# Performance work log

Hardware: AMD Instinct MI355X
Metric: run time of the kernel (lower is better)

## Reference

```python
import jax, jax.numpy as jnp
import numpy as np

D_MODEL = 1024
N_HEADS = 16
DEPTH = D_MODEL // N_HEADS
B, S = 2, 2048


def layer_norm(x, gamma, beta):
    # Faithful to the torch module: unbiased std (ddof=1), eps added to std.
    mean = jnp.mean(x, axis=-1, keepdims=True)
    std = jnp.std(x, axis=-1, ddof=1, keepdims=True)
    return gamma * ((x - mean) / (std + 1e-6)) + beta


def setup_inputs() -> dict:
    key = jax.random.key(0)
    ks = jax.random.split(key, 12)
    sc = 0.02
    x = jax.random.normal(ks[0], (B, S, D_MODEL), jnp.float32)
    mask = jnp.triu(jnp.ones((S, S), jnp.float32), k=1)  # 1 where masked (future)
    return {
        "x": x,
        "mask": mask,
        "wq_w": jax.random.normal(ks[1], (D_MODEL, D_MODEL), jnp.float32) * sc,
        "wq_b": jnp.zeros((D_MODEL,), jnp.float32),
        "wk_w": jax.random.normal(ks[2], (D_MODEL, D_MODEL), jnp.float32) * sc,
        "wk_b": jnp.zeros((D_MODEL,), jnp.float32),
        "wv_w": jax.random.normal(ks[3], (D_MODEL, D_MODEL), jnp.float32) * sc,
        "wv_b": jnp.zeros((D_MODEL,), jnp.float32),
        "dense_w": jax.random.normal(ks[4], (D_MODEL, D_MODEL), jnp.float32) * sc,
        "dense_b": jnp.zeros((D_MODEL,), jnp.float32),
        "gamma1": jnp.ones((D_MODEL,), jnp.float32),
        "beta1": jnp.zeros((D_MODEL,), jnp.float32),
        "gamma2": jnp.ones((D_MODEL,), jnp.float32),
        "beta2": jnp.zeros((D_MODEL,), jnp.float32),
        "fc_w": jax.random.normal(ks[5], (4 * D_MODEL, D_MODEL), jnp.float32) * sc,
        "proj_w": jax.random.normal(ks[6], (D_MODEL, 4 * D_MODEL), jnp.float32) * sc,
    }


def reference(x, mask, wq_w, wq_b, wk_w, wk_b, wv_w, wv_b, dense_w, dense_b,
              gamma1, beta1, gamma2, beta2, fc_w, proj_w):
    # x: [B,S,D]. Dropout is identity in eval.
    xn = layer_norm(x, gamma1, beta1)

    def split(h):  # [B,S,D] -> [B,H,S,depth]
        return h.reshape(B, S, N_HEADS, DEPTH).transpose(0, 2, 1, 3)

    q = split(xn @ wq_w.T + wq_b)
    k = split(xn @ wk_w.T + wk_b)
    v = split(xn @ wv_w.T + wv_b)

    scores = jnp.einsum("bhqd,bhkd->bhqk", q, k) / jnp.sqrt(
        jnp.asarray(DEPTH, jnp.float32))
    scores = scores + mask * -1e9
    attn = jax.nn.softmax(scores, axis=-1)
    ctx = jnp.einsum("bhqk,bhkd->bhqd", attn, v)
    ctx = ctx.transpose(0, 2, 1, 3).reshape(B, S, D_MODEL)
    attn_out = ctx @ dense_w.T + dense_b

    # Residual adds the *normed* x (faithful to the original ordering).
    h = xn + attn_out
    hn = layer_norm(h, gamma2, beta2)

    ff = jax.nn.gelu(hn @ fc_w.T, approximate=False) @ proj_w.T
    return hn + ff
```

## Files before the change

kernel.cpp:

```cpp
#include <hip/hip_runtime.h>
#include <math.h>

typedef __bf16 bf16;
typedef __attribute__((ext_vector_type(2))) __bf16 bf16x2;
typedef __attribute__((ext_vector_type(4))) __bf16 bf16x4;
typedef __attribute__((ext_vector_type(8))) __bf16 bf16x8;
typedef __attribute__((ext_vector_type(4))) float f32x4;

#define D_MODEL 1024
#define NH 16
#define DP 64
#define BB 2
#define SEQ 2048
#define TOK 4096
#define FFD 4096
#define AST 72

__device__ __forceinline__ void async16(bf16* lds, const bf16* g) {
    __builtin_amdgcn_global_load_lds(
        (__attribute__((address_space(1))) void*)g,
        (__attribute__((address_space(3))) void*)lds, 16, 0, 0);
}

__device__ __forceinline__ f32x4 mfma16(bf16x8 a, bf16x8 b, f32x4 c) {
    return __builtin_amdgcn_mfma_f32_16x16x32_bf16(a, b, c, 0, 0, 0);
}

__device__ __forceinline__ void xcd_swz(int& bx, int& by, int& bz) {
    const int gx = gridDim.x, gy = gridDim.y;
    const int nwg = gx * gy * gridDim.z;
    const int orig = (blockIdx.z * gy + blockIdx.y) * gx + blockIdx.x;
    const int q = nwg >> 3;
    const int n = (orig & 7) * q + (orig >> 3);
    bx = n % gx;
    const int r = n / gx;
    by = r % gy;
    bz = r / gy;
}

struct CvtArgs {
    const float4* in[6];
    bf16x4* out[6];
};
__global__ __launch_bounds__(256) void cvt_all(CvtArgs a)
{
    const int i = blockIdx.x * 256 + threadIdx.x;
    int seg, idx;
    if (i < (1 << 20)) { seg = i >> 18; idx = i & ((1 << 18) - 1); }
    else {
        const int j = i - (1 << 20);
        seg = 4 + (j >> 20); idx = j & ((1 << 20) - 1);
    }
    const float4 v = a.in[seg][idx];
    bf16x4 o; o[0] = (bf16)v.x; o[1] = (bf16)v.y; o[2] = (bf16)v.z; o[3] = (bf16)v.w;
    a.out[seg][idx] = o;
}

template<typename TIN>
__global__ __launch_bounds__(256) void ln_kernel(
    const TIN* __restrict__ in, const float* __restrict__ g,
    const float* __restrict__ be, bf16* __restrict__ out)
{
    const size_t row = blockIdx.x;
    const int t = threadIdx.x;
    const TIN* x = in + row * D_MODEL;

    float v0, v1, v2, v3;
    if constexpr (sizeof(TIN) == 4) {
        const float4 xv = *(const float4*)(x + t * 4);
        v0 = xv.x; v1 = xv.y; v2 = xv.z; v3 = xv.w;
    } else {
        const bf16x4 xv = *(const bf16x4*)(x + t * 4);
        v0 = (float)xv[0]; v1 = (float)xv[1]; v2 = (float)xv[2]; v3 = (float)xv[3];
    }
    float s  = v0 + v1 + v2 + v3;
    float ss = v0*v0 + v1*v1 + v2*v2 + v3*v3;
    #pragma unroll
    for (int off = 32; off > 0; off >>= 1) {
        s  += __shfl_down(s, off);
        ss += __shfl_down(ss, off);
    }
    __shared__ float rs[4], rss[4];
    if ((t & 63) == 0) { rs[t >> 6] = s; rss[t >> 6] = ss; }
    __syncthreads();
    const float S  = rs[0] + rs[1] + rs[2] + rs[3];
    const float SS = rss[0] + rss[1] + rss[2] + rss[3];
    const float mean = S * (1.0f / 1024.0f);
    const float var  = fmaxf((SS - S * mean) * (1.0f / 1023.0f), 0.0f);
    const float inv  = 1.0f / (sqrtf(var) + 1e-6f);

    const float4 gv = *(const float4*)(g  + t * 4);
    const float4 bv = *(const float4*)(be + t * 4);
    bf16x4 ov;
    ov[0] = (bf16)(gv.x * ((v0 - mean) * inv) + bv.x);
    ov[1] = (bf16)(gv.y * ((v1 - mean) * inv) + bv.y);
    ov[2] = (bf16)(gv.z * ((v2 - mean) * inv) + bv.z);
    ov[3] = (bf16)(gv.w * ((v3 - mean) * inv) + bv.w);
    *(bf16x4*)(out + row * D_MODEL + t * 4) = ov;
}

template<int EPI, typename TOUT>
__global__ __launch_bounds__(256, 2) void gemm_bt(
    const bf16* __restrict__ A, const bf16* __restrict__ W,
    const float* __restrict__ bias, const bf16* res,
    TOUT* C, int M, int N, int K, float scale)
{
    int bx, by, bz; xcd_swz(bx, by, bz);
    __shared__ __align__(16) bf16 As[2][128 * 32];
    __shared__ __align__(16) bf16 Bs[2][128 * 32];
    const int t = threadIdx.x;
    const int w = t >> 6, lane = t & 63;
    const int fr = lane & 15, quad = lane >> 4;
    const int m0 = by * 128, n0 = bx * 128;
    const int wm = (w >> 1) * 64, wn = (w & 1) * 64;

    const f32x4 z = {0.f, 0.f, 0.f, 0.f};
    f32x4 acc[4][4];
    #pragma unroll
    for (int i = 0; i < 4; ++i)
        #pragma unroll
        for (int j = 0; j < 4; ++j) acc[i][j] = z;

    const int nk = K >> 5;
    const int srow = t >> 2, ssub = t & 3;

    #pragma unroll
    for (int call = 0; call < 2; ++call) {
        const int row = call * 64 + srow;
        async16(&As[0][(size_t)(call * 256 + w * 64) * 8],
                A + (size_t)(m0 + row) * K + ssub * 8);
        async16(&Bs[0][(size_t)(call * 256 + w * 64) * 8],
                W + (size_t)(n0 + row) * K + ssub * 8);
    }
    __syncthreads();

    for (int kt = 0; kt < nk; ++kt) {
        const int cur = kt & 1;
        if (kt + 1 < nk) {
            const int k0 = (kt + 1) << 5;
            #pragma unroll
            for (int call = 0; call < 2; ++call) {
                const int row = call * 64 + srow;
                async16(&As[cur ^ 1][(size_t)(call * 256 + w * 64) * 8],
                        A + (size_t)(m0 + row) * K + k0 + ssub * 8);
                async16(&Bs[cur ^ 1][(size_t)(call * 256 + w * 64) * 8],
                        W + (size_t)(n0 + row) * K + k0 + ssub * 8);
            }
        }
        bf16x8 af[4], bfr[4];
        #pragma unroll
        for (int i = 0; i < 4; ++i)
            af[i] = *(const bf16x8*)&As[cur][(wm + i * 16 + fr) * 32 + quad * 8];
        #pragma unroll
        for (int j = 0; j < 4; ++j)
            bfr[j] = *(const bf16x8*)&Bs[cur][(wn + j * 16 + fr) * 32 + quad * 8];
        #pragma unroll
        for (int i = 0; i < 4; ++i)
            #pragma unroll
            for (int j = 0; j < 4; ++j)
                acc[i][j] = mfma16(af[i], bfr[j], acc[i][j]);
        __syncthreads();
    }

    #pragma unroll
    for (int i = 0; i < 4; ++i) {
        #pragma unroll
        for (int j = 0; j < 4; ++j) {
            #pragma unroll
            for (int r = 0; r < 4; ++r) {
                const int m = m0 + wm + i * 16 + quad * 4 + r;
                const int n = n0 + wn + j * 16 + fr;
                float v = acc[i][j][r];
                if (EPI == 1) {
                    v += bias[n];
                    v += (float)res[(size_t)m * N + n];
                    C[(size_t)m * N + n] = (TOUT)v;
                } else if (EPI == 2) {
                    v = 0.5f * v * (1.0f + erff(v * 0.70710678118f));
                    C[(size_t)m * N + n] = (TOUT)v;
                } else {
                    v += (float)res[(size_t)m * N + n];
                    C[(size_t)m * N + n] = (TOUT)v;
                }
            }
        }
    }
}

template<int EPI, typename TOUT>
__global__ __launch_bounds__(256, 2) void gemm_bt64(
    const bf16* __restrict__ A, const bf16* __restrict__ W,
    const float* __restrict__ bias, const bf16* res,
    TOUT* C, TOUT* Cb, int M, int N, int K, int kchunk)
{
    int bx, by, bz; xcd_swz(bx, by, bz);
    __shared__ __align__(16) bf16 As[2][128 * 32];
    __shared__ __align__(16) bf16 Bs[2][64 * 32];
    const int t = threadIdx.x;
    const int w = t >> 6, lane = t & 63;
    const int fr = lane & 15, quad = lane >> 4;
    const int m0 = by * 128, n0 = bx * 64;
    const int kbase = bz * kchunk;
    TOUT* Cz = (EPI == 4 && bz) ? Cb : C;
    const int wm = (w >> 1) * 64, wn = (w & 1) * 32;

    const f32x4 z = {0.f, 0.f, 0.f, 0.f};
    f32x4 acc[4][2];
    #pragma unroll
    for (int i = 0; i < 4; ++i)
        #pragma unroll
        for (int j = 0; j < 2; ++j) acc[i][j] = z;

    const int nk = kchunk >> 5;
    const int srow = t >> 2, ssub = t & 3;

    #pragma unroll
    for (int call = 0; call < 2; ++call) {
        const int row = call * 64 + srow;
        async16(&As[0][(size_t)(call * 256 + w * 64) * 8],
                A + (size_t)(m0 + row) * K + kbase + ssub * 8);
    }
    async16(&Bs[0][(size_t)(w * 64) * 8],
            W + (size_t)(n0 + srow) * K + kbase + ssub * 8);
    __syncthreads();

    for (int kt = 0; kt < nk; ++kt) {
        const int cur = kt & 1;
        if (kt + 1 < nk) {
            const int k0 = kbase + ((kt + 1) << 5);
            #pragma unroll
            for (int call = 0; call < 2; ++call) {
                const int row = call * 64 + srow;
                async16(&As[cur ^ 1][(size_t)(call * 256 + w * 64) * 8],
                        A + (size_t)(m0 + row) * K + k0 + ssub * 8);
            }
            async16(&Bs[cur ^ 1][(size_t)(w * 64) * 8],
                    W + (size_t)(n0 + srow) * K + k0 + ssub * 8);
        }
        bf16x8 af[4], bfr[2];
        #pragma unroll
        for (int i = 0; i < 4; ++i)
            af[i] = *(const bf16x8*)&As[cur][(wm + i * 16 + fr) * 32 + quad * 8];
        #pragma unroll
        for (int j = 0; j < 2; ++j)
            bfr[j] = *(const bf16x8*)&Bs[cur][(wn + j * 16 + fr) * 32 + quad * 8];
        #pragma unroll
        for (int i = 0; i < 4; ++i)
            #pragma unroll
            for (int j = 0; j < 2; ++j)
                acc[i][j] = mfma16(af[i], bfr[j], acc[i][j]);
        __syncthreads();
    }

    #pragma unroll
    for (int i = 0; i < 4; ++i) {
        #pragma unroll
        for (int j = 0; j < 2; ++j) {
            #pragma unroll
            for (int r = 0; r < 4; ++r) {
                const int m = m0 + wm + i * 16 + quad * 4 + r;
                const int n = n0 + wn + j * 16 + fr;
                float v = acc[i][j][r];
                if (EPI == 1) {
                    v += bias[n];
                    v += (float)res[(size_t)m * N + n];
                    Cz[(size_t)m * N + n] = (TOUT)v;
                } else if (EPI == 4) {
                    Cz[(size_t)m * N + n] = (TOUT)v;
                } else {
                    v += (float)res[(size_t)m * N + n];
                    Cz[(size_t)m * N + n] = (TOUT)v;
                }
            }
        }
    }
}

__global__ __launch_bounds__(256) void combine_add(
    const float4* __restrict__ p1, const bf16x4* __restrict__ res,
    float4* __restrict__ out)
{
    const int i = blockIdx.x * 256 + threadIdx.x;
    const float4 a = out[i], b = p1[i];
    const bf16x4 r = res[i];
    float4 o;
    o.x = a.x + b.x + (float)r[0];
    o.y = a.y + b.y + (float)r[1];
    o.z = a.z + b.z + (float)r[2];
    o.w = a.w + b.w + (float)r[3];
    out[i] = o;
}

__global__ __launch_bounds__(256, 2) void gemm_qkv(
    const bf16* __restrict__ A,
    const bf16* __restrict__ wq, const bf16* __restrict__ wk,
    const bf16* __restrict__ wvv,
    const float* __restrict__ bq, const float* __restrict__ bk,
    const float* __restrict__ bv,
    bf16* __restrict__ outq, bf16* __restrict__ outk, bf16* __restrict__ outv)
{
    int bx, by, bz; xcd_swz(bx, by, bz);
    const int sel = bx >> 3;
    const bf16* W = (sel == 0) ? wq : ((sel == 1) ? wk : wvv);
    const float* bias = (sel == 0) ? bq : ((sel == 1) ? bk : bv);
    bf16* C = (sel == 0) ? outq : ((sel == 1) ? outk : outv);
    const float scale = (sel == 0) ? 0.125f : 1.0f;
    const int K = D_MODEL;

    __shared__ __align__(16) bf16 As[2][128 * 32];
    __shared__ __align__(16) bf16 Bs[2][128 * 32];
    const int t = threadIdx.x;
    const int w = t >> 6, lane = t & 63;
    const int fr = lane & 15, quad = lane >> 4;
    const int m0 = by * 128, n0 = (bx & 7) * 128;
    const int wm = (w >> 1) * 64, wn = (w & 1) * 64;

    const f32x4 z = {0.f, 0.f, 0.f, 0.f};
    f32x4 acc[4][4];
    #pragma unroll
    for (int i = 0; i < 4; ++i)
        #pragma unroll
        for (int j = 0; j < 4; ++j) acc[i][j] = z;

    const int nk = D_MODEL >> 5;
    const int srow = t >> 2, ssub = t & 3;

    #pragma unroll
    for (int call = 0; call < 2; ++call) {
        const int row = call * 64 + srow;
        async16(&As[0][(size_t)(call * 256 + w * 64) * 8],
                A + (size_t)(m0 + row) * K + ssub * 8);
        async16(&Bs[0][(size_t)(call * 256 + w * 64) * 8],
                W + (size_t)(n0 + row) * K + ssub * 8);
    }
    __syncthreads();

    for (int kt = 0; kt < nk; ++kt) {
        const int cur = kt & 1;
        if (kt + 1 < nk) {
            const int k0 = (kt + 1) << 5;
            #pragma unroll
            for (int call = 0; call < 2; ++call) {
                const int row = call * 64 + srow;
                async16(&As[cur ^ 1][(size_t)(call * 256 + w * 64) * 8],
                        A + (size_t)(m0 + row) * K + k0 + ssub * 8);
                async16(&Bs[cur ^ 1][(size_t)(call * 256 + w * 64) * 8],
                        W + (size_t)(n0 + row) * K + k0 + ssub * 8);
            }
        }
        bf16x8 af[4], bfr[4];
        #pragma unroll
        for (int i = 0; i < 4; ++i)
            af[i] = *(const bf16x8*)&As[cur][(wm + i * 16 + fr) * 32 + quad * 8];
        #pragma unroll
        for (int j = 0; j < 4; ++j)
            bfr[j] = *(const bf16x8*)&Bs[cur][(wn + j * 16 + fr) * 32 + quad * 8];
        #pragma unroll
        for (int i = 0; i < 4; ++i)
            #pragma unroll
            for (int j = 0; j < 4; ++j)
                acc[i][j] = mfma16(af[i], bfr[j], acc[i][j]);
        __syncthreads();
    }

    #pragma unroll
    for (int i = 0; i < 4; ++i)
        #pragma unroll
        for (int j = 0; j < 4; ++j)
            #pragma unroll
            for (int r = 0; r < 4; ++r) {
                const int m = m0 + wm + i * 16 + quad * 4 + r;
                const int n = n0 + wn + j * 16 + fr;
                const float vv = (acc[i][j][r] + bias[n]) * scale;
                const int b = m >> 11, s = m & 2047, h = n >> 6, d = n & 63;
                C[(((size_t)(b * NH + h)) * SEQ + s) * DP + d] = (bf16)vv;
            }
}

__global__ __launch_bounds__(256, 3) void attn_kernel(
    const bf16* __restrict__ q, const bf16* __restrict__ k,
    const bf16* __restrict__ v, bf16* __restrict__ ctx)
{
    __shared__ __align__(16) bf16 Ks[2][64 * AST];
    __shared__ __align__(16) bf16 VsT[2][64 * AST];
    __shared__ __align__(16) bf16 Ps[4][16 * AST];
    const int t = threadIdx.x, wv = t >> 6, lane = t & 63;
    const int fr = lane & 15, quad = lane >> 4;
    const int id = blockIdx.y * 32 + blockIdx.x;
    const int nid = (id & 7) * 128 + (id >> 3);
    const int bh = nid >> 5;
    const int qt = 31 - (nid & 31);
    const size_t base = (size_t)bh * SEQ * DP;
    const int b = bh >> 4, hh = bh & 15;
    const f32x4 z = {0.f, 0.f, 0.f, 0.f};
    const int krow = t >> 2, kd0 = (t & 3) * 16;
    const int pp = t & 31, c0 = (t >> 5) * 8;

    const int q0 = qt * 64, qr0 = q0 + wv * 16;
    const int nkt = qt + 1;
    const int myq = qr0 + fr;

    bf16x8 qf[2];
    #pragma unroll
    for (int c = 0; c < 2; ++c)
        qf[c] = *(const bf16x8*)(q + base + (size_t)myq * DP + c * 32 + quad * 8);

    bf16x8 k0r, k1r, v0r, v1r;
    {
        const bf16* kp = k + base + (size_t)krow * DP + kd0;
        k0r = *(const bf16x8*)kp; k1r = *(const bf16x8*)(kp + 8);
        const bf16* vp = v + base + (size_t)(2 * pp) * DP + c0;
        v0r = *(const bf16x8*)vp; v1r = *(const bf16x8*)(vp + DP);
    }

    f32x4 o[4] = {z, z, z, z};
    float mi = -1e30f, li = 0.f;

    for (int kt = 0; kt < nkt; ++kt) {
        const int cur = kt & 1;
        const int kk0 = kt * 64;
        *(bf16x8*)&Ks[cur][krow * AST + kd0]     = k0r;
        *(bf16x8*)&Ks[cur][krow * AST + kd0 + 8] = k1r;
        #pragma unroll
        for (int j = 0; j < 8; ++j) {
            bf16x2 pr; pr[0] = v0r[j]; pr[1] = v1r[j];
            *(bf16x2*)&VsT[cur][(c0 + j) * AST + 2 * pp] = pr;
        }
        __syncthreads();
        if (kt + 1 < nkt) {
            const bf16* kp = k + base + (size_t)(kk0 + 64 + krow) * DP + kd0;
            k0r = *(const bf16x8*)kp; k1r = *(const bf16x8*)(kp + 8);
            const bf16* vp = v + base + (size_t)(kk0 + 64 + 2 * pp) * DP + c0;
            v0r = *(const bf16x8*)vp; v1r = *(const bf16x8*)(vp + DP);
        }

        f32x4 sa[4] = {z, z, z, z};
        __builtin_amdgcn_s_setprio(1);
        #pragma unroll
        for (int nb = 0; nb < 4; ++nb)
            #pragma unroll
            for (int c = 0; c < 2; ++c) {
                const bf16x8 kf = *(const bf16x8*)&Ks[cur][(nb * 16 + fr) * AST + c * 32 + quad * 8];
                sa[nb] = mfma16(kf, qf[c], sa[nb]);
            }
        __builtin_amdgcn_s_setprio(0);

        float p[4][4];
        float rmax = -1e30f;
        #pragma unroll
        for (int nb = 0; nb < 4; ++nb)
            #pragma unroll
            for (int r = 0; r < 4; ++r) {
                const int key = kk0 + nb * 16 + quad * 4 + r;
                float sv = sa[nb][r];
                if (key > myq) sv += -1e9f;
                p[nb][r] = sv;
                rmax = fmaxf(rmax, sv);
            }
        rmax = fmaxf(rmax, __shfl_xor(rmax, 16));
        rmax = fmaxf(rmax, __shfl_xor(rmax, 32));

        const float nm = fmaxf(mi, rmax);
        const float alpha = __expf(mi - nm);
        mi = nm;
        float ps = 0.f;
        #pragma unroll
        for (int nb = 0; nb < 4; ++nb)
            #pragma unroll
            for (int r = 0; r < 4; ++r) {
                const float e = __expf(p[nb][r] - nm);
                p[nb][r] = e;
                ps += e;
            }
        ps += __shfl_xor(ps, 16);
        ps += __shfl_xor(ps, 32);
        li = li * alpha + ps;

        float ab[4];
        #pragma unroll
        for (int r = 0; r < 4; ++r) ab[r] = __shfl(alpha, quad * 4 + r, 16);
        #pragma unroll
        for (int db = 0; db < 4; ++db)
            #pragma unroll
            for (int r = 0; r < 4; ++r) o[db][r] *= ab[r];

        #pragma unroll
        for (int nb = 0; nb < 4; ++nb) {
            bf16x4 pw;
            pw[0] = (bf16)p[nb][0]; pw[1] = (bf16)p[nb][1];
            pw[2] = (bf16)p[nb][2]; pw[3] = (bf16)p[nb][3];
            *(bf16x4*)&Ps[wv][fr * AST + nb * 16 + quad * 4] = pw;
        }

        bf16x8 pf[2];
        #pragma unroll
        for (int c = 0; c < 2; ++c)
            pf[c] = *(const bf16x8*)&Ps[wv][fr * AST + c * 32 + quad * 8];
        __builtin_amdgcn_s_setprio(1);
        #pragma unroll
        for (int db = 0; db < 4; ++db)
            #pragma unroll
            for (int c = 0; c < 2; ++c) {
                const bf16x8 vf = *(const bf16x8*)&VsT[cur][(db * 16 + fr) * AST + c * 32 + quad * 8];
                o[db] = mfma16(pf[c], vf, o[db]);
            }
        __builtin_amdgcn_s_setprio(0);
    }

    float lir[4];
    #pragma unroll
    for (int r = 0; r < 4; ++r) lir[r] = __shfl(li, quad * 4 + r, 16);
    #pragma unroll
    for (int db = 0; db < 4; ++db)
        #pragma unroll
        for (int r = 0; r < 4; ++r) {
            const int qrow = qr0 + quad * 4 + r;
            const int d = db * 16 + fr;
            ctx[((size_t)(b * SEQ + qrow)) * D_MODEL + hh * DP + d] =
                (bf16)(o[db][r] / lir[r]);
        }
}

extern "C" void kernel_launch(void* const* d_in, const int* in_sizes, int n_in,
                              void* d_out, int out_size, void* d_ws, size_t ws_size,
                              hipStream_t stream) {
    const float* x       = (const float*)d_in[0];
    const float* wq_w    = (const float*)d_in[2];
    const float* wq_b    = (const float*)d_in[3];
    const float* wk_w    = (const float*)d_in[4];
    const float* wk_b    = (const float*)d_in[5];
    const float* wv_w    = (const float*)d_in[6];
    const float* wv_b    = (const float*)d_in[7];
    const float* dense_w = (const float*)d_in[8];
    const float* dense_b = (const float*)d_in[9];
    const float* gamma1  = (const float*)d_in[10];
    const float* beta1   = (const float*)d_in[11];
    const float* gamma2  = (const float*)d_in[12];
    const float* beta2   = (const float*)d_in[13];
    const float* fc_w    = (const float*)d_in[14];
    const float* proj_w  = (const float*)d_in[15];
    float* out = (float*)d_out;

    bf16* ws = (bf16*)d_ws;
    const size_t M1 = (size_t)1 << 20;
    bf16* xn   = ws;
    bf16* qb   = ws + 4 * M1;
    bf16* kb   = ws + 8 * M1;
    bf16* vb   = ws + 12 * M1;
    bf16* ctx  = ws + 16 * M1;
    bf16* ff1  = qb;
    bf16* wqc  = ws + 20 * M1;
    bf16* wkc  = ws + 21 * M1;
    bf16* wvc  = ws + 22 * M1;
    bf16* wdc  = ws + 23 * M1;
    bf16* fcc  = ws + 24 * M1;
    bf16* prjc = ws + 28 * M1;
    bf16* h = xn, *hn = xn;
    float* part1 = (float*)(ws + 20 * M1);

    CvtArgs ca;
    ca.in[0] = (const float4*)wq_w;    ca.out[0] = (bf16x4*)wqc;
    ca.in[1] = (const float4*)wk_w;    ca.out[1] = (bf16x4*)wkc;
    ca.in[2] = (const float4*)wv_w;    ca.out[2] = (bf16x4*)wvc;
    ca.in[3] = (const float4*)dense_w; ca.out[3] = (bf16x4*)wdc;
    ca.in[4] = (const float4*)fc_w;    ca.out[4] = (bf16x4*)fcc;
    ca.in[5] = (const float4*)proj_w;  ca.out[5] = (bf16x4*)prjc;
    cvt_all<<<12288, 256, 0, stream>>>(ca);

    ln_kernel<float><<<TOK, 256, 0, stream>>>(x, gamma1, beta1, xn);
    gemm_qkv<<<dim3(24, 32), 256, 0, stream>>>(xn, wqc, wkc, wvc,
                                               wq_b, wk_b, wv_b, qb, kb, vb);
    attn_kernel<<<dim3(32, BB * NH), 256, 0, stream>>>(qb, kb, vb, ctx);
    gemm_bt64<1, bf16><<<dim3(16, 32), 256, 0, stream>>>(
        ctx, wdc, dense_b, xn, h, (bf16*)nullptr, TOK, D_MODEL, D_MODEL, D_MODEL);
    ln_kernel<bf16><<<TOK, 256, 0, stream>>>(h, gamma2, beta2, hn);
    gemm_bt<2, bf16><<<dim3(32, 32), 256, 0, stream>>>(hn, fcc, nullptr, nullptr, ff1,
                                                       TOK, FFD, D_MODEL, 1.0f);
    gemm_bt64<4, float><<<dim3(16, 32, 2), 256, 0, stream>>>(
        ff1, prjc, nullptr, nullptr, out, part1, TOK, D_MODEL, FFD, FFD / 2);
    combine_add<<<4096, 256, 0, stream>>>(
        (const float4*)part1, (const bf16x4*)hn, (float4*)out);
}
```

Before: 375.8 us.

## Skip mask on full tiles, lazy softmax rescale, transpose PV MFMA output

Key tiles that lie entirely below the causal diagonal now skip the per-element mask compare. The online-softmax running max is only updated, and the accumulator rescaled, when some lane's row max grows by more than a threshold; otherwise the stale max is kept, as in FlashAttention-4-style lazy rescaling. The PV MFMA operands are swapped so each lane owns its query row's outputs. This removes the alpha/li shuffles and allows vectorized bf16x4 stores of ctx. The lazy rescale accepts bounded exp growth, which is safe only while the threshold keeps values within fp32/bf16 range.

```diff
diff --git a/kernel.cpp b/kernel.cpp
--- a/kernel.cpp
+++ b/kernel.cpp
@@ -447,42 +447,52 @@
 
         float p[4][4];
         float rmax = -1e30f;
-        #pragma unroll
-        for (int nb = 0; nb < 4; ++nb)
-            #pragma unroll
-            for (int r = 0; r < 4; ++r) {
-                const int key = kk0 + nb * 16 + quad * 4 + r;
-                float sv = sa[nb][r];
-                if (key > myq) sv += -1e9f;
-                p[nb][r] = sv;
-                rmax = fmaxf(rmax, sv);
-            }
+        if (kk0 + 63 > qr0) {
+            #pragma unroll
+            for (int nb = 0; nb < 4; ++nb)
+                #pragma unroll
+                for (int r = 0; r < 4; ++r) {
+                    const int key = kk0 + nb * 16 + quad * 4 + r;
+                    float sv = sa[nb][r];
+                    if (key > myq) sv += -1e9f;
+                    p[nb][r] = sv;
+                    rmax = fmaxf(rmax, sv);
+                }
+        } else {
+            #pragma unroll
+            for (int nb = 0; nb < 4; ++nb)
+                #pragma unroll
+                for (int r = 0; r < 4; ++r) {
+                    p[nb][r] = sa[nb][r];
+                    rmax = fmaxf(rmax, sa[nb][r]);
+                }
+        }
         rmax = fmaxf(rmax, __shfl_xor(rmax, 16));
         rmax = fmaxf(rmax, __shfl_xor(rmax, 32));
 
-        const float nm = fmaxf(mi, rmax);
-        const float alpha = __expf(mi - nm);
-        mi = nm;
+        const bool need = !__all(rmax - mi <= 8.0f);
+        if (need) {
+            const float nm = fmaxf(mi, rmax);
+            const float alpha = __expf(mi - nm);
+            mi = nm;
+            li *= alpha;
+            #pragma unroll
+            for (int db = 0; db < 4; ++db)
+                #pragma unroll
+                for (int r = 0; r < 4; ++r) o[db][r] *= alpha;
+        }
         float ps = 0.f;
         #pragma unroll
         for (int nb = 0; nb < 4; ++nb)
             #pragma unroll
             for (int r = 0; r < 4; ++r) {
-                const float e = __expf(p[nb][r] - nm);
+                const float e = __expf(p[nb][r] - mi);
                 p[nb][r] = e;
                 ps += e;
             }
         ps += __shfl_xor(ps, 16);
         ps += __shfl_xor(ps, 32);
-        li = li * alpha + ps;
-
-        float ab[4];
-        #pragma unroll
-        for (int r = 0; r < 4; ++r) ab[r] = __shfl(alpha, quad * 4 + r, 16);
-        #pragma unroll
-        for (int db = 0; db < 4; ++db)
-            #pragma unroll
-            for (int r = 0; r < 4; ++r) o[db][r] *= ab[r];
+        li += ps;
 
         #pragma unroll
         for (int nb = 0; nb < 4; ++nb) {
@@ -502,23 +512,20 @@
             #pragma unroll
             for (int c = 0; c < 2; ++c) {
                 const bf16x8 vf = *(const bf16x8*)&VsT[cur][(db * 16 + fr) * AST + c * 32 + quad * 8];
-                o[db] = mfma16(pf[c], vf, o[db]);
+                o[db] = mfma16(vf, pf[c], o[db]);
             }
         __builtin_amdgcn_s_setprio(0);
     }
 
-    float lir[4];
-    #pragma unroll
-    for (int r = 0; r < 4; ++r) lir[r] = __shfl(li, quad * 4 + r, 16);
-    #pragma unroll
-    for (int db = 0; db < 4; ++db)
-        #pragma unroll
-        for (int r = 0; r < 4; ++r) {
-            const int qrow = qr0 + quad * 4 + r;
-            const int d = db * 16 + fr;
-            ctx[((size_t)(b * SEQ + qrow)) * D_MODEL + hh * DP + d] =
-                (bf16)(o[db][r] / lir[r]);
-        }
+    const float inv_li = 1.0f / li;
+    #pragma unroll
+    for (int db = 0; db < 4; ++db) {
+        bf16x4 ov;
+        #pragma unroll
+        for (int r = 0; r < 4; ++r) ov[r] = (bf16)(o[db][r] * inv_li);
+        const int d = db * 16 + quad * 4;
+        *(bf16x4*)&ctx[((size_t)(b * SEQ + myq)) * D_MODEL + hh * DP + d] = ov;
+    }
 }
 
 extern "C" void kernel_launch(void* const* d_in, const int* in_sizes, int n_in,
```

Result: faster. 367.5 us (median of 3 runs) (-2.2%).
